# Optimization experiments

Measured on AMD Instinct MI355X. Metric: run time of the kernel, lower is better.

The kernel has to match this reference:

```python
import jax, jax.numpy as jnp
import numpy as np
from jax import lax

D_MODEL = 200
N_LAYER = 12
NHEADS = 8
HEADDIM = 50
D_STATE = 64
D_INNER = 2 * D_MODEL            # 400
CONV_DIM = D_INNER + 2 * D_STATE  # 528 (ngroups=1)
D_IN_PROJ = 2 * D_INNER + 2 * D_STATE + NHEADS  # 936
D_CONV = 4
EPS = 1e-5


def rmsnorm(x, w):
    v = jnp.mean(jnp.square(x), axis=-1, keepdims=True)
    return x * lax.rsqrt(v + EPS) * w


def groupnorm(x, groups, g, b):
    B, C, H, W = x.shape
    xg = x.reshape(B, groups, C // groups, H, W)
    mu = jnp.mean(xg, axis=(2, 3, 4), keepdims=True)
    var = jnp.mean(jnp.square(xg - mu), axis=(2, 3, 4), keepdims=True)
    xn = ((xg - mu) * lax.rsqrt(var + EPS)).reshape(B, C, H, W)
    return xn * g[:, None, None] + b[:, None, None]


def patch_embed(x, pe_conv_w, proj_in_w, gn_g, gn_b, spec_w):
    b, c, l, d = x.shape
    # time path: 'b c l d' -> (b, 1, c*l, d), conv -> (b, 25, c*l, 8)
    time_x = x.reshape(b, 1, c * l, d)
    t = lax.conv_general_dilated(time_x, proj_in_w, (1, 25), ((0, 0), (24, 24)),
                                 dimension_numbers=('NCHW', 'OIHW', 'NCHW'))
    t = jax.nn.gelu(groupnorm(t, 5, gn_g, gn_b), approximate=False)
    time_emb = t.transpose(0, 2, 1, 3).reshape(b, c, l, D_MODEL)
    # freq path: rfft over patch dim, norm='forward'
    spec = jnp.abs(jnp.fft.rfft(x, axis=-1, norm='forward'))  # (b,c,l,101)
    spec_emb = jnp.einsum('bclf,df->bcld', spec, spec_w)
    patch = time_emb + spec_emb
    # depthwise 7x7 positional conv over (d, c, l)
    pos = lax.conv_general_dilated(patch.transpose(0, 3, 1, 2), pe_conv_w, (1, 1),
                                   ((3, 3), (3, 3)),
                                   dimension_numbers=('NCHW', 'OIHW', 'NCHW'),
                                   feature_group_count=D_MODEL)
    return patch + pos.transpose(0, 2, 3, 1)


def ssd_scan(xh, dt, B, C, A, D):
    # xh: (b,l,h,p)  dt: (b,l,h)  B,C: (b,l,n)  A,D: (h,)
    b, l, h, p = xh.shape

    def step(state, inp):
        x_t, dt_t, B_t, C_t = inp
        dA = jnp.exp(dt_t * A)  # (b,h)
        state = state * dA[:, :, None, None] + \
            (dt_t[:, :, None, None] * x_t[:, :, :, None]) * B_t[:, None, None, :]
        y = jnp.einsum('bhpn,bn->bhp', state, C_t)
        return state, y

    state0 = jnp.zeros((b, h, p, D_STATE), xh.dtype)
    _, ys = lax.scan(step, state0,
                     (xh.transpose(1, 0, 2, 3), dt.transpose(1, 0, 2),
                      B.transpose(1, 0, 2), C.transpose(1, 0, 2)))
    return ys.transpose(1, 0, 2, 3) + xh * D[None, None, :, None]


def mamba2(u, in_w, conv_w, conv_b, dt_bias, A_log, D, gn_w, out_w):
    b, l, _ = u.shape
    zxbcdt = u @ in_w.T  # (b,l,936)
    z = zxbcdt[..., :D_INNER]
    xBC = zxbcdt[..., D_INNER:D_INNER + CONV_DIM]
    dt = jax.nn.softplus(zxbcdt[..., D_INNER + CONV_DIM:] + dt_bias)  # (b,l,8)
    # causal depthwise conv1d, kernel 4
    xc = lax.conv_general_dilated(xBC.transpose(0, 2, 1), conv_w, (1,), ((D_CONV - 1, 0),),
                                  dimension_numbers=('NCH', 'OIH', 'NCH'),
                                  feature_group_count=CONV_DIM)
    xBC = jax.nn.silu((xc + conv_b[:, None]).transpose(0, 2, 1))
    x = xBC[..., :D_INNER].reshape(b, l, NHEADS, HEADDIM)
    Bm = xBC[..., D_INNER:D_INNER + D_STATE]
    Cm = xBC[..., D_INNER + D_STATE:]
    y = ssd_scan(x, dt, Bm, Cm, -jnp.exp(A_log), D).reshape(b, l, D_INNER)
    y = rmsnorm(y * jax.nn.silu(z), gn_w)  # RMSNormGated, norm_before_gate=False
    return y @ out_w.T


@jax.checkpoint
def layer(hidden, residual, norm_w, in_w, conv_w, conv_b, dt_bias, A_log, D, gn_w, out_w):
    residual = hidden + residual
    hidden = mamba2(rmsnorm(residual, norm_w), in_w, conv_w, conv_b, dt_bias, A_log, D, gn_w, out_w)
    return hidden, residual


def forward(x, pe_conv_w, proj_in_w, gn_g, gn_b, spec_w, norm_w, in_proj_w, conv_w, conv_b,
            dt_bias, A_log, D, gnorm_w, out_proj_w, norm_f_w, head_w, head_b):
    b, c, l, d = x.shape
    hidden = patch_embed(x, pe_conv_w, proj_in_w, gn_g, gn_b, spec_w).reshape(b, c * l, d)
    residual = jnp.zeros_like(hidden)
    for i in range(N_LAYER):
        hidden, residual = layer(hidden, residual, norm_w[i], in_proj_w[i], conv_w[i],
                                 conv_b[i], dt_bias[i], A_log[i], D[i], gnorm_w[i], out_proj_w[i])
    hidden = rmsnorm(hidden + residual, norm_f_w).reshape(b, c, l, d)
    return hidden @ head_w.T + head_b


def setup_inputs():
    key = jax.random.key(0)
    ks = jax.random.split(key, 12)
    B, CH, L, P = 16, 19, 30, 200

    def g(k, shape, scale):
        return jax.random.normal(k, shape, jnp.float32) * scale

    dt = jax.random.uniform(ks[8], (N_LAYER, NHEADS), jnp.float32, 1e-3, 0.1)
    return {
        'x': g(ks[0], (B, CH, L, P), 1.0),
        'pe_conv_w': g(ks[1], (D_MODEL, 1, 7, 7), 0.15),
        'proj_in_w': g(ks[2], (25, 1, 1, 49), 0.14),
        'gn_g': jnp.ones(25, jnp.float32),
        'gn_b': jnp.zeros(25, jnp.float32),
        'spec_w': g(ks[3], (D_MODEL, 101), 0.1),
        'norm_w': jnp.ones((N_LAYER, D_MODEL), jnp.float32),
        'in_proj_w': g(ks[4], (N_LAYER, D_IN_PROJ, D_MODEL), 0.07),
        'conv_w': g(ks[5], (N_LAYER, CONV_DIM, 1, D_CONV), 0.4),
        'conv_b': jnp.zeros((N_LAYER, CONV_DIM), jnp.float32),
        'dt_bias': jnp.log(jnp.expm1(dt)),
        'A_log': jnp.log(jax.random.uniform(ks[9], (N_LAYER, NHEADS), jnp.float32, 1.0, 16.0)),
        'D': jnp.ones((N_LAYER, NHEADS), jnp.float32),
        'gnorm_w': jnp.ones((N_LAYER, D_INNER), jnp.float32),
        'out_proj_w': g(ks[6], (N_LAYER, D_MODEL, D_INNER), 0.05),
        'norm_f_w': jnp.ones(D_MODEL, jnp.float32),
        'head_w': g(ks[7], (D_MODEL, D_MODEL), 0.07),
        'head_b': jnp.zeros(D_MODEL, jnp.float32),
    }


def reference(x, pe_conv_w, proj_in_w, gn_g, gn_b, spec_w, norm_w, in_proj_w, conv_w, conv_b,
              dt_bias, A_log, D, gnorm_w, out_proj_w, norm_f_w, head_w, head_b):
    return forward(x, pe_conv_w, proj_in_w, gn_g, gn_b, spec_w, norm_w, in_proj_w, conv_w,
                   conv_b, dt_bias, A_log, D, gnorm_w, out_proj_w, norm_f_w, head_w, head_b)
```

## Files before the change

### kernel.cpp

```cpp
#include <hip/hip_runtime.h>
#include <hip/hip_bf16.h>
#include <math.h>

#define D_MODEL   200
#define N_LAYER   12
#define NHEADS    8
#define HEADDIM   50
#define D_STATE   64
#define D_INNER   400
#define CONV_DIM  528
#define D_IN_PROJ 936
#define D_CONV    4
#define EPS       1e-5f

#define BATCH 16
#define CH    19
#define LLEN  30
#define SEQ   570
#define NTOK  9120
#define NFREQ 101

typedef __attribute__((ext_vector_type(8))) short s8v;
typedef __attribute__((ext_vector_type(4))) float f32x4;

__device__ __forceinline__ short f2bf(float f) {
    unsigned u = __float_as_uint(f);
    u += 0x7FFFu + ((u >> 16) & 1u);
    return (short)(u >> 16);
}

__global__ __launch_bounds__(256) void gemm_bf16(
    const short* __restrict__ A, const short* __restrict__ W,
    const float* __restrict__ bias, const float* __restrict__ rowscale,
    float* __restrict__ C, int M, int N, int Kp, int accum)
{
    __shared__ __align__(16) short As[128][40];
    __shared__ __align__(16) short Ws[128][40];

    int bm = blockIdx.y * 128;
    int bn = blockIdx.x * 128;
    int tid = threadIdx.x;
    int lane = tid & 63;
    int wv = tid >> 6;
    int wm = wv & 1, wn = wv >> 1;
    int lm = lane & 15, lg = lane >> 4;

    int sr = tid >> 1;
    int sh_ = (tid & 1) * 16;

    f32x4 acc[4][4];
#pragma unroll
    for (int i = 0; i < 4; i++)
#pragma unroll
        for (int j = 0; j < 4; j++) acc[i][j] = (f32x4)0.f;

    for (int k0 = 0; k0 < Kp; k0 += 32) {
        {
            s8v v0 = (s8v)0, v1 = (s8v)0;
            if (bm + sr < M) {
                const short* ga = A + (size_t)(bm + sr) * Kp + k0 + sh_;
                v0 = *(const s8v*)ga;
                v1 = *(const s8v*)(ga + 8);
            }
            *(s8v*)&As[sr][sh_] = v0;
            *(s8v*)&As[sr][sh_ + 8] = v1;
        }
        {
            s8v v0 = (s8v)0, v1 = (s8v)0;
            if (bn + sr < N) {
                const short* gw = W + (size_t)(bn + sr) * Kp + k0 + sh_;
                v0 = *(const s8v*)gw;
                v1 = *(const s8v*)(gw + 8);
            }
            *(s8v*)&Ws[sr][sh_] = v0;
            *(s8v*)&Ws[sr][sh_ + 8] = v1;
        }
        __syncthreads();

        s8v af[4], bf[4];
#pragma unroll
        for (int i = 0; i < 4; i++)
            af[i] = *(const s8v*)&As[wm * 64 + i * 16 + lm][lg * 8];
#pragma unroll
        for (int j = 0; j < 4; j++)
            bf[j] = *(const s8v*)&Ws[wn * 64 + j * 16 + lm][lg * 8];
#pragma unroll
        for (int i = 0; i < 4; i++)
#pragma unroll
            for (int j = 0; j < 4; j++)
                acc[i][j] = __builtin_amdgcn_mfma_f32_16x16x32_bf16(
                    af[i], bf[j], acc[i][j], 0, 0, 0);
        __syncthreads();
    }

#pragma unroll
    for (int j = 0; j < 4; j++) {
        int n = bn + wn * 64 + j * 16 + lm;
        if (n >= N) continue;
        float bv = bias ? bias[n] : 0.f;
#pragma unroll
        for (int i = 0; i < 4; i++) {
            int mbase = bm + wm * 64 + i * 16 + lg * 4;
#pragma unroll
            for (int r = 0; r < 4; r++) {
                int m = mbase + r;
                if (m >= M) continue;
                size_t idx = (size_t)m * N + n;
                float v = acc[i][j][r];
                if (rowscale) v *= rowscale[m];
                v += bv;
                if (accum) v += C[idx];
                C[idx] = v;
            }
        }
    }
}

__global__ __launch_bounds__(256) void gemm_nt(
    const float* __restrict__ A, const float* __restrict__ W,
    const float* __restrict__ bias, float* __restrict__ C,
    int M, int N, int K, int accum)
{
    const int BM = 128, BK = 16;
    __shared__ float As[16][BM + 4];
    __shared__ float Ws[16][BM + 4];

    int bm = blockIdx.y * BM;
    int bn = blockIdx.x * BM;
    int tid = threadIdx.x;
    int lr = tid >> 1;
    int lc = (tid & 1) * 8;
    int tx = tid & 15;
    int ty = tid >> 4;

    float acc[8][8];
#pragma unroll
    for (int i = 0; i < 8; i++)
#pragma unroll
        for (int j = 0; j < 8; j++) acc[i][j] = 0.f;

    for (int k0 = 0; k0 < K; k0 += BK) {
#pragma unroll
        for (int i = 0; i < 8; i++) {
            int gr = bm + lr, gk = k0 + lc + i;
            As[lc + i][lr] = (gr < M && gk < K) ? A[(size_t)gr * K + gk] : 0.f;
        }
#pragma unroll
        for (int i = 0; i < 8; i++) {
            int gr = bn + lr, gk = k0 + lc + i;
            Ws[lc + i][lr] = (gr < N && gk < K) ? W[(size_t)gr * K + gk] : 0.f;
        }
        __syncthreads();
#pragma unroll
        for (int kk = 0; kk < BK; kk++) {
            float a[8], bv[8];
#pragma unroll
            for (int i = 0; i < 8; i++) a[i] = As[kk][ty * 8 + i];
#pragma unroll
            for (int j = 0; j < 8; j++) bv[j] = Ws[kk][tx * 8 + j];
#pragma unroll
            for (int i = 0; i < 8; i++)
#pragma unroll
                for (int j = 0; j < 8; j++)
                    acc[i][j] = fmaf(a[i], bv[j], acc[i][j]);
        }
        __syncthreads();
    }

#pragma unroll
    for (int i = 0; i < 8; i++) {
        int gm = bm + ty * 8 + i;
        if (gm >= M) continue;
#pragma unroll
        for (int j = 0; j < 8; j++) {
            int gn = bn + tx * 8 + j;
            if (gn >= N) continue;
            float v = acc[i][j];
            if (bias) v += bias[gn];
            if (accum) v += C[(size_t)gm * N + gn];
            C[(size_t)gm * N + gn] = v;
        }
    }
}

__global__ __launch_bounds__(256) void cast_pad_kernel(
    const float* __restrict__ src, short* __restrict__ dst,
    int R, int K, int Kp)
{
    int idx = blockIdx.x * 256 + threadIdx.x;
    if (idx >= R * Kp) return;
    int r = idx / Kp, k = idx - r * Kp;
    dst[idx] = (k < K) ? f2bf(src[(size_t)r * K + k]) : (short)0;
}

__global__ __launch_bounds__(256) void time_conv_kernel(
    const float* __restrict__ x, const float* __restrict__ pw,
    float* __restrict__ traw)
{
    int br = blockIdx.x;
    __shared__ float xr[200];
    if (threadIdx.x < 200) xr[threadIdx.x] = x[(size_t)br * 200 + threadIdx.x];
    __syncthreads();
    if (threadIdx.x < 200) {
        int oc = threadIdx.x >> 3, j = threadIdx.x & 7;
        int start = j * 25 - 24;
        float acc = 0.f;
#pragma unroll
        for (int k = 0; k < 49; k++) {
            int d = start + k;
            if (d >= 0 && d < 200) acc = fmaf(xr[d], pw[oc * 49 + k], acc);
        }
        int b = br / SEQ, row = br % SEQ;
        traw[(((size_t)b * 25 + oc) * SEQ + row) * 8 + j] = acc;
    }
}

__global__ __launch_bounds__(256) void gn_stats_kernel(
    const float* __restrict__ traw, float* __restrict__ stats)
{
    int bg = blockIdx.x;
    int b = bg / 5, g = bg % 5;
    const float* base = traw + ((size_t)b * 25 + g * 5) * SEQ * 8;
    float s = 0.f, q = 0.f;
    for (int i = threadIdx.x; i < 5 * SEQ * 8; i += 256) {
        float v = base[i];
        s += v; q = fmaf(v, v, q);
    }
    __shared__ float rs[4], rq[4];
    int lane = threadIdx.x & 63, w = threadIdx.x >> 6;
#pragma unroll
    for (int o = 32; o; o >>= 1) { s += __shfl_xor(s, o, 64); q += __shfl_xor(q, o, 64); }
    if (lane == 0) { rs[w] = s; rq[w] = q; }
    __syncthreads();
    if (threadIdx.x == 0) {
        float S = rs[0] + rs[1] + rs[2] + rs[3];
        float Q = rq[0] + rq[1] + rq[2] + rq[3];
        float inv = 1.f / (5.f * SEQ * 8.f);
        float mean = S * inv;
        float var = Q * inv - mean * mean;
        stats[bg * 2] = mean;
        stats[bg * 2 + 1] = rsqrtf(var + EPS);
    }
}

__global__ __launch_bounds__(256) void gn_gelu_kernel(
    const float* __restrict__ traw, const float* __restrict__ stats,
    const float* __restrict__ gn_g, const float* __restrict__ gn_b,
    float* __restrict__ patch)
{
    int idx = blockIdx.x * 256 + threadIdx.x;
    if (idx >= NTOK * 200) return;
    int d = idx % 200;
    int row = (idx / 200) % SEQ;
    int b = idx / (200 * SEQ);
    int oc = d >> 3, j = d & 7;
    float v = traw[(((size_t)b * 25 + oc) * SEQ + row) * 8 + j];
    int g = oc / 5;
    float mean = stats[(b * 5 + g) * 2];
    float rstd = stats[(b * 5 + g) * 2 + 1];
    v = (v - mean) * rstd * gn_g[oc] + gn_b[oc];
    float ge = 0.5f * v * (1.f + erff(v * 0.70710678118654752f));
    patch[idx] = ge;
}

__global__ __launch_bounds__(256) void dft_init_kernel(float* __restrict__ CS)
{
    int idx = blockIdx.x * 256 + threadIdx.x;
    if (idx >= 202 * 200) return;
    int f = idx / 200, d = idx % 200;
    int fr = (f < NFREQ) ? f : (f - NFREQ);
    int m = (fr * d) % 200;
    float ang = -6.283185307179586f * (float)m * (1.f / 200.f);
    CS[idx] = (f < NFREQ) ? cosf(ang) : sinf(ang);
}

__global__ __launch_bounds__(256) void dft_init_bf_kernel(short* __restrict__ CS)
{
    int idx = blockIdx.x * 256 + threadIdx.x;
    if (idx >= 202 * 224) return;
    int f = idx / 224, d = idx - f * 224;
    short out = 0;
    if (d < 200) {
        int fr = (f < NFREQ) ? f : (f - NFREQ);
        int m = (fr * d) % 200;
        float ang = -6.283185307179586f * (float)m * (1.f / 200.f);
        out = f2bf((f < NFREQ) ? cosf(ang) : sinf(ang));
    }
    CS[idx] = out;
}

__global__ __launch_bounds__(256) void mag_kernel(
    const float* __restrict__ cs_out, float* __restrict__ magv)
{
    int idx = blockIdx.x * 256 + threadIdx.x;
    if (idx >= NTOK * NFREQ) return;
    int m = idx / NFREQ, f = idx % NFREQ;
    float re = cs_out[(size_t)m * 202 + f];
    float im = cs_out[(size_t)m * 202 + NFREQ + f];
    magv[idx] = sqrtf(re * re + im * im) * 0.005f;
}

__global__ __launch_bounds__(256) void mag_bf_kernel(
    const float* __restrict__ cs_out, short* __restrict__ magv)
{
    int idx = blockIdx.x * 256 + threadIdx.x;
    if (idx >= NTOK * 128) return;
    int m = idx >> 7, f = idx & 127;
    short out = 0;
    if (f < NFREQ) {
        float re = cs_out[(size_t)m * 202 + f];
        float im = cs_out[(size_t)m * 202 + NFREQ + f];
        out = f2bf(sqrtf(re * re + im * im) * 0.005f);
    }
    magv[idx] = out;
}

__global__ __launch_bounds__(256) void pe_conv3_kernel(
    const float* __restrict__ patch, const float* __restrict__ pw,
    float* __restrict__ hidden)
{
    int b = blockIdx.x, dc = blockIdx.y, ct = blockIdx.z;
    int d0 = dc * 16, c0 = ct * 4;
    __shared__ float pl[10 * 30 * 16];
    __shared__ float wl[49 * 16];
    int tid = threadIdx.x;
    int dd = tid & 15;
    int d = d0 + dd;

    for (int i = tid; i < 10 * 30 * 16; i += 256) {
        int ddl = i & 15, r = i >> 4;
        int l = r % 30, cr = r / 30;
        int cc = c0 + cr - 3, dl = d0 + ddl;
        pl[i] = (cc >= 0 && cc < CH && dl < 200)
                    ? patch[((size_t)(b * CH + cc) * LLEN + l) * 200 + dl] : 0.f;
    }
    for (int i = tid; i < 49 * 16; i += 256) {
        int k = i >> 4, dl = d0 + (i & 15);
        wl[i] = (dl < 200) ? pw[(size_t)dl * 49 + k] : 0.f;
    }
    __syncthreads();

    float wreg[49];
#pragma unroll
    for (int k = 0; k < 49; k++) wreg[k] = wl[k * 16 + dd];

    for (int o = tid; o < 4 * 30 * 16; o += 256) {
        int r2 = o >> 4;
        int l = r2 % 30, ci = r2 / 30;
        int c = c0 + ci;
        if (c >= CH) continue;
        float acc = pl[((ci + 3) * 30 + l) * 16 + dd];
#pragma unroll
        for (int i = 0; i < 7; i++) {
#pragma unroll
            for (int j = 0; j < 7; j++) {
                int ll = l + j - 3;
                if (ll < 0 || ll >= LLEN) continue;
                acc = fmaf(pl[((ci + i) * 30 + ll) * 16 + dd], wreg[i * 7 + j], acc);
            }
        }
        if (d < 200) hidden[((size_t)(b * CH + c) * LLEN + l) * 200 + d] = acc;
    }
}

__global__ __launch_bounds__(64) void add_rmsnorm_kernel(
    const float* __restrict__ hidden, float* __restrict__ residual,
    const float* __restrict__ wn, float* __restrict__ u,
    short* __restrict__ ubf, int first)
{
    int m = blockIdx.x;
    int lane = threadIdx.x;
    const float* hr = hidden + (size_t)m * 200;
    float* rr = residual + (size_t)m * 200;
    float v[4];
    float ss = 0.f;
#pragma unroll
    for (int i = 0; i < 4; i++) {
        int k = lane + i * 64;
        float xv = 0.f;
        if (k < 200) {
            xv = hr[k] + (first ? 0.f : rr[k]);
            rr[k] = xv;
        }
        v[i] = xv;
        ss = fmaf(xv, xv, ss);
    }
#pragma unroll
    for (int o = 32; o; o >>= 1) ss += __shfl_xor(ss, o, 64);
    float rstd = rsqrtf(ss * (1.f / 200.f) + EPS);
#pragma unroll
    for (int i = 0; i < 4; i++) {
        int k = lane + i * 64;
        float val = v[i] * rstd * ((k < 200) ? wn[k] : 0.f);
        if (k < 200 && u) u[(size_t)m * 200 + k] = val;
        if (ubf) {
            if (k < 200) ubf[(size_t)m * 224 + k] = f2bf(val);
            else if (k < 224) ubf[(size_t)m * 224 + k] = 0;
        }
    }
}

__global__ __launch_bounds__(256) void norm_dt_kernel(
    const float* __restrict__ hidden, float* __restrict__ residual,
    const float* __restrict__ wn, short* __restrict__ ubf,
    const float* __restrict__ Win, const float* __restrict__ dt_bias,
    float* __restrict__ dtb, int layer, int first)
{
    int m = blockIdx.x;
    int tid = threadIdx.x;
    __shared__ float su[200];
    __shared__ float rs[4];
    float xv = 0.f;
    if (tid < 200) {
        xv = hidden[(size_t)m * 200 + tid] + (first ? 0.f : residual[(size_t)m * 200 + tid]);
        residual[(size_t)m * 200 + tid] = xv;
    }
    float ss = xv * xv;
#pragma unroll
    for (int o = 32; o; o >>= 1) ss += __shfl_xor(ss, o, 64);
    int lane = tid & 63, w = tid >> 6;
    if (lane == 0) rs[w] = ss;
    __syncthreads();
    float rstd = rsqrtf((rs[0] + rs[1] + rs[2] + rs[3]) * (1.f / 200.f) + EPS);
    if (tid < 200) {
        float val = xv * rstd * wn[tid];
        su[tid] = val;
        ubf[(size_t)m * 224 + tid] = f2bf(val);
    } else if (tid < 224) {
        ubf[(size_t)m * 224 + tid] = 0;
    }
    __syncthreads();
    int h = tid >> 5, l = tid & 31;
    const float* wr = Win + (size_t)layer * D_IN_PROJ * 200 + (size_t)(928 + h) * 200;
    float s = 0.f;
    for (int k = l; k < 200; k += 32) s = fmaf(su[k], wr[k], s);
    s += __shfl_xor(s, 16, 32);
    s += __shfl_xor(s, 8, 32);
    s += __shfl_xor(s, 4, 32);
    s += __shfl_xor(s, 2, 32);
    s += __shfl_xor(s, 1, 32);
    if (l == 0) {
        float raw = s + dt_bias[layer * NHEADS + h];
        dtb[(size_t)m * NHEADS + h] = (raw > 20.f) ? raw : log1pf(expf(raw));
    }
}

__global__ __launch_bounds__(256) void dt_gemv_kernel(
    const float* __restrict__ u, const float* __restrict__ Win,
    const float* __restrict__ dt_bias, float* __restrict__ dtb, int layer)
{
    int tid = threadIdx.x;
    int tok = blockIdx.x * 4 + (tid >> 6);
    int head = (tid >> 3) & 7;
    int l8 = tid & 7;
    const float* ur = u + (size_t)tok * 200;
    const float* wr = Win + (size_t)layer * D_IN_PROJ * 200 + (size_t)(928 + head) * 200;
    float s = 0.f;
    for (int k = l8; k < 200; k += 8) s = fmaf(ur[k], wr[k], s);
    s += __shfl_xor(s, 1, 64);
    s += __shfl_xor(s, 2, 64);
    s += __shfl_xor(s, 4, 64);
    if (l8 == 0) {
        float raw = s + dt_bias[layer * NHEADS + head];
        dtb[(size_t)tok * NHEADS + head] = (raw > 20.f) ? raw : log1pf(expf(raw));
    }
}

__global__ __launch_bounds__(256) void dtconv2_kernel(
    const float* __restrict__ zxbcdt, const float* __restrict__ cw,
    const float* __restrict__ cb, float* __restrict__ xBC, int layer)
{
    int b = blockIdx.x, tt = blockIdx.y;
    int t0 = tt * 8;
    __shared__ float zs[11][528];
    const float* cwl = cw + (size_t)layer * CONV_DIM * 4;
    const float* cbl = cb + (size_t)layer * CONV_DIM;
    for (int i = threadIdx.x; i < 11 * 528; i += 256) {
        int r = i / 528, ch = i - r * 528;
        int t = t0 - 3 + r;
        zs[r][ch] = (t >= 0 && t < SEQ)
                        ? zxbcdt[(size_t)(b * SEQ + t) * D_IN_PROJ + D_INNER + ch] : 0.f;
    }
    __syncthreads();
    for (int o = threadIdx.x; o < 8 * 528; o += 256) {
        int tr = o / 528, ch = o - tr * 528;
        int t = t0 + tr;
        if (t >= SEQ) continue;
        float acc = cbl[ch];
#pragma unroll
        for (int k = 0; k < 4; k++)
            acc = fmaf(zs[tr + k][ch], cwl[ch * 4 + k], acc);
        xBC[(size_t)(b * SEQ + t) * CONV_DIM + ch] = acc / (1.f + __expf(-acc));
    }
}

__global__ __launch_bounds__(256) void ssd_state12_kernel(
    const float* __restrict__ xBC, const float* __restrict__ dtb,
    const float* __restrict__ A_log, float* __restrict__ Sbuf,
    float* __restrict__ Pd, int layer, int lchunk, int nchunk)
{
    int b = blockIdx.x, c = blockIdx.y, bz = blockIdx.z;
    int tid = threadIdx.x;
    int w = tid >> 6, lane = tid & 63;
    int h = bz * 4 + w;
    int t0 = c * lchunk;
    float A = -expf(A_log[layer * NHEADS + h]);

    __shared__ __align__(16) short Bt[64 * 64];
    __shared__ __align__(16) short Xw[4][64 * 64];

    for (int i = tid; i < 512; i += 256) ((s8v*)Bt)[i] = (s8v)0;
#pragma unroll
    for (int ww = 0; ww < 4; ww++)
        for (int i = tid; i < 512; i += 256) ((s8v*)Xw[ww])[i] = (s8v)0;
    __syncthreads();

    float dtv = 0.f;
    if (lane < lchunk) dtv = dtb[(size_t)(b * SEQ + t0 + lane) * NHEADS + h];
    float lc = dtv * A;
#pragma unroll
    for (int o = 1; o < 64; o <<= 1) {
        float v = __shfl_up(lc, o, 64);
        if (lane >= o) lc += v;
    }
    float lcTot = __shfl(lc, lchunk - 1, 64);
    float wdec = __expf(lcTot - lc) * dtv;

    for (int idx = tid; idx < lchunk * 64; idx += 256) {
        int s = idx >> 6, n = idx & 63;
        float v = xBC[(size_t)(b * SEQ + t0 + s) * CONV_DIM + D_INNER + n];
        Bt[n * 64 + s] = f2bf(v);
    }
    for (int idx = lane; idx < lchunk * HEADDIM; idx += 64) {
        int s = idx / HEADDIM, p = idx - s * HEADDIM;
        float ws = __shfl(wdec, s, 64);
        float v = xBC[(size_t)(b * SEQ + t0 + s) * CONV_DIM + h * HEADDIM + p] * ws;
        Xw[w][p * 64 + s] = f2bf(v);
    }
    __syncthreads();

    int lm = lane & 15, lg = lane >> 4;
    f32x4 acc[4][4];
#pragma unroll
    for (int i = 0; i < 4; i++)
#pragma unroll
        for (int j = 0; j < 4; j++) acc[i][j] = (f32x4)0.f;

#pragma unroll
    for (int k0 = 0; k0 < 64; k0 += 32) {
        s8v af[4], bf[4];
#pragma unroll
        for (int i = 0; i < 4; i++)
            af[i] = *(const s8v*)&Xw[w][(i * 16 + lm) * 64 + k0 + lg * 8];
#pragma unroll
        for (int j = 0; j < 4; j++)
            bf[j] = *(const s8v*)&Bt[(j * 16 + lm) * 64 + k0 + lg * 8];
#pragma unroll
        for (int i = 0; i < 4; i++)
#pragma unroll
            for (int j = 0; j < 4; j++)
                acc[i][j] = __builtin_amdgcn_mfma_f32_16x16x32_bf16(
                    af[i], bf[j], acc[i][j], 0, 0, 0);
    }

    float* Sb = Sbuf + ((size_t)((b * NHEADS + h) * nchunk + c)) * (HEADDIM * 64);
#pragma unroll
    for (int i = 0; i < 4; i++) {
        int pbase = i * 16 + lg * 4;
#pragma unroll
        for (int r = 0; r < 4; r++) {
            int p = pbase + r;
            if (p >= HEADDIM) continue;
#pragma unroll
            for (int j = 0; j < 4; j++) {
                int n = j * 16 + lm;
                Sb[(size_t)p * 64 + n] = acc[i][j][r];
            }
        }
    }
    if (lane == 0) Pd[(b * NHEADS + h) * nchunk + c] = __expf(lcTot);
}

__global__ __launch_bounds__(512) void ssd_state_kernel(
    const float* __restrict__ xBC, const float* __restrict__ dtb,
    const float* __restrict__ A_log, float* __restrict__ Sbuf,
    float* __restrict__ Pd, int layer, int lchunk, int nchunk)
{
    int b = blockIdx.x, c = blockIdx.y;
    int tid = threadIdx.x;
    int h = tid >> 6, p = tid & 63;
    float A = -expf(A_log[layer * NHEADS + h]);

    __shared__ float sh[2][544];
    int t0 = c * lchunk, tend = t0 + lchunk;

    {
        const float* base = xBC + (size_t)(b * SEQ + t0) * CONV_DIM;
        sh[0][tid] = base[tid];
        if (tid < 24) {
            int e2 = 512 + tid;
            sh[0][e2] = (e2 < 528) ? base[e2]
                                   : dtb[(size_t)(b * SEQ + t0) * NHEADS + (e2 - 528)];
        }
    }
    __syncthreads();

    float s[64];
#pragma unroll
    for (int n = 0; n < 64; n++) s[n] = 0.f;
    float pacc = 1.f;

    for (int t = t0; t < tend; t++) {
        int cur = (t - t0) & 1, nxt = cur ^ 1;
        float pf0 = 0.f, pf1 = 0.f;
        if (t + 1 < tend) {
            const float* base = xBC + (size_t)(b * SEQ + t + 1) * CONV_DIM;
            pf0 = base[tid];
            if (tid < 24) {
                int e2 = 512 + tid;
                pf1 = (e2 < 528) ? base[e2]
                                 : dtb[(size_t)(b * SEQ + t + 1) * NHEADS + (e2 - 528)];
            }
        }
        float dtv = sh[cur][528 + h];
        float xp  = (p < HEADDIM) ? sh[cur][h * HEADDIM + p] : 0.f;
        float dA = __expf(dtv * A);
        float u  = dtv * xp;
        pacc *= dA;
        const float4* B4 = (const float4*)&sh[cur][D_INNER];
#pragma unroll
        for (int n4 = 0; n4 < 16; n4++) {
            float4 bq = B4[n4];
            s[4 * n4 + 0] = fmaf(s[4 * n4 + 0], dA, u * bq.x);
            s[4 * n4 + 1] = fmaf(s[4 * n4 + 1], dA, u * bq.y);
            s[4 * n4 + 2] = fmaf(s[4 * n4 + 2], dA, u * bq.z);
            s[4 * n4 + 3] = fmaf(s[4 * n4 + 3], dA, u * bq.w);
        }
        if (t + 1 < tend) {
            sh[nxt][tid] = pf0;
            if (tid < 24) sh[nxt][512 + tid] = pf1;
        }
        __syncthreads();
    }

    if (p < HEADDIM) {
        float* Sb = Sbuf + ((size_t)((b * NHEADS + h) * nchunk + c)) * (HEADDIM * 64)
                    + p * 64;
#pragma unroll
        for (int n4 = 0; n4 < 16; n4++)
            ((float4*)Sb)[n4] = make_float4(s[4 * n4], s[4 * n4 + 1],
                                            s[4 * n4 + 2], s[4 * n4 + 3]);
    }
    if (p == 0) Pd[(b * NHEADS + h) * nchunk + c] = pacc;
}

__global__ __launch_bounds__(256) void ssd_scan2b_kernel(
    float* __restrict__ Sbuf, const float* __restrict__ Pd, int nchunk)
{
    int bh = blockIdx.x;
    int e = blockIdx.y * 256 + threadIdx.x;
    if (e >= HEADDIM * 64) return;
    float* base = Sbuf + (size_t)bh * nchunk * (HEADDIM * 64) + e;
    const float* pd = Pd + bh * nchunk;
    float cur = 0.f;
    for (int c = 0; c < nchunk; c++) {
        float l = base[(size_t)c * (HEADDIM * 64)];
        base[(size_t)c * (HEADDIM * 64)] = cur;
        cur = fmaf(pd[c], cur, l);
    }
}

__global__ __launch_bounds__(256) void ssd_out7_kernel(
    const float* __restrict__ xBC, const float* __restrict__ dtb,
    const float* __restrict__ zxbcdt, const float* __restrict__ A_log,
    const float* __restrict__ Dv, const float* __restrict__ Sbuf,
    const float* __restrict__ gw, short* __restrict__ ybf,
    float* __restrict__ ssq, int layer, int lchunk, int nchunk)
{
    int b = blockIdx.x, c = blockIdx.y, bz = blockIdx.z;
    int tid = threadIdx.x;
    int hl = tid >> 6, p = tid & 63;
    int h = bz * 4 + hl;
    float A = -expf(A_log[layer * NHEADS + h]);
    float Dh = Dv[layer * NHEADS + h];
    float gval = (p < HEADDIM) ? gw[(size_t)layer * D_INNER + h * HEADDIM + p] : 0.f;

    __shared__ __align__(16) float sBC[4][2][256];
    int t0 = c * lchunk;
    int npairs = lchunk >> 1;

    const float* xb  = xBC + (size_t)(b * SEQ + t0) * CONV_DIM;
    const float* zb  = zxbcdt + (size_t)(b * SEQ + t0) * D_IN_PROJ;
    const float* dtp = dtb + (size_t)(b * SEQ + t0) * NHEADS + h;

    int ldtok = p >> 5;
    int ldf4  = 100 + (p & 31);
    int ldoff = ldtok * 128 + ((p & 31) << 2);

    float4 gv;
    gv = ((const float4*)(xb + (size_t)ldtok * CONV_DIM))[ldf4];
    *(float4*)&sBC[hl][0][ldoff] = gv;
    float nx0 = (p < HEADDIM) ? xb[h * HEADDIM + p] : 0.f;
    float nx1 = (p < HEADDIM) ? xb[CONV_DIM + h * HEADDIM + p] : 0.f;
    float nz0 = (p < HEADDIM) ? zb[h * HEADDIM + p] : 0.f;
    float nz1 = (p < HEADDIM) ? zb[D_IN_PROJ + h * HEADDIM + p] : 0.f;
    float ndt0 = dtp[0];
    float ndt1 = dtp[NHEADS];
    if (npairs > 1)
        gv = ((const float4*)(xb + (size_t)(2 + ldtok) * CONV_DIM))[ldf4];

    float s[64];
    if (p < HEADDIM) {
        const float* Sb = Sbuf + ((size_t)((b * NHEADS + h) * nchunk + c)) * (HEADDIM * 64)
                          + p * 64;
#pragma unroll
        for (int n4 = 0; n4 < 16; n4++) {
            float4 v = ((const float4*)Sb)[n4];
            s[4 * n4] = v.x; s[4 * n4 + 1] = v.y; s[4 * n4 + 2] = v.z; s[4 * n4 + 3] = v.w;
        }
    } else {
#pragma unroll
        for (int n = 0; n < 64; n++) s[n] = 0.f;
    }

    for (int i = 0; i < npairs; i++) {
        int buf = i & 1;
        int t = t0 + 2 * i;
        float x0 = nx0, x1 = nx1, z0 = nz0, z1 = nz1, dt0 = ndt0, dt1 = ndt1;
        if (i + 1 < npairs) {
            *(float4*)&sBC[hl][buf ^ 1][ldoff] = gv;
            const float* xn = xb + (size_t)(2 * (i + 1)) * CONV_DIM;
            const float* zn = zb + (size_t)(2 * (i + 1)) * D_IN_PROJ;
            nx0 = (p < HEADDIM) ? xn[h * HEADDIM + p] : 0.f;
            nx1 = (p < HEADDIM) ? xn[CONV_DIM + h * HEADDIM + p] : 0.f;
            nz0 = (p < HEADDIM) ? zn[h * HEADDIM + p] : 0.f;
            nz1 = (p < HEADDIM) ? zn[D_IN_PROJ + h * HEADDIM + p] : 0.f;
            ndt0 = dtp[(size_t)(2 * (i + 1)) * NHEADS];
            ndt1 = dtp[(size_t)(2 * (i + 1) + 1) * NHEADS];
            if (i + 2 < npairs)
                gv = ((const float4*)(xb + (size_t)(2 * (i + 2) + ldtok) * CONV_DIM))[ldf4];
        }
#pragma unroll
        for (int k = 0; k < 2; k++) {
            float dtv = k ? dt1 : dt0;
            float xp  = k ? x1 : x0;
            float zv  = k ? z1 : z0;
            float dA = __expf(dtv * A);
            float u  = dtv * xp;
            const float4* B4 = (const float4*)&sBC[hl][buf][k * 128];
            const float4* C4 = (const float4*)&sBC[hl][buf][k * 128 + 64];
            float y0 = 0.f, y1 = 0.f, y2 = 0.f, y3 = 0.f;
#pragma unroll
            for (int n4 = 0; n4 < 16; n4++) {
                float4 bq = B4[n4];
                float4 cq = C4[n4];
                float t0v = fmaf(s[4 * n4 + 0], dA, u * bq.x);
                float t1v = fmaf(s[4 * n4 + 1], dA, u * bq.y);
                float t2v = fmaf(s[4 * n4 + 2], dA, u * bq.z);
                float t3v = fmaf(s[4 * n4 + 3], dA, u * bq.w);
                s[4 * n4 + 0] = t0v; s[4 * n4 + 1] = t1v;
                s[4 * n4 + 2] = t2v; s[4 * n4 + 3] = t3v;
                y0 = fmaf(t0v, cq.x, y0);
                y1 = fmaf(t1v, cq.y, y1);
                y2 = fmaf(t2v, cq.z, y2);
                y3 = fmaf(t3v, cq.w, y3);
            }
            float g0 = 0.f;
            if (p < HEADDIM) {
                float yv = fmaf(xp, Dh, (y0 + y1) + (y2 + y3));
                g0 = yv * (zv / (1.f + __expf(-zv)));
            }
            size_t row0 = (size_t)(b * SEQ + t + k) * 416;
            if (p < HEADDIM) {
                ybf[row0 + h * HEADDIM + p] = f2bf(g0 * gval);
            } else {
                int widx = h * 14 + (p - HEADDIM);
                if (widx < 16) ybf[row0 + 400 + widx] = 0;
            }
            float gs0 = g0 * g0;
#pragma unroll
            for (int o = 32; o; o >>= 1) gs0 += __shfl_xor(gs0, o, 64);
            if (p == 0) ssq[(size_t)(b * SEQ + t + k) * NHEADS + h] = gs0;
        }
    }
}

__global__ __launch_bounds__(256) void rstd_kernel(
    const float* __restrict__ ssq, float* __restrict__ rstdb)
{
    int m = blockIdx.x * 256 + threadIdx.x;
    if (m >= NTOK) return;
    const float4* q = (const float4*)(ssq + (size_t)m * NHEADS);
    float4 a = q[0], bq = q[1];
    float tot = ((a.x + a.y) + (a.z + a.w)) + ((bq.x + bq.y) + (bq.z + bq.w));
    rstdb[m] = rsqrtf(tot * (1.f / D_INNER) + EPS);
}

__global__ __launch_bounds__(512) void ssd_out_kernel(
    const float* __restrict__ xBC, const float* __restrict__ dtb,
    const float* __restrict__ A_log, const float* __restrict__ Dv,
    const float* __restrict__ Sbuf, float* __restrict__ y,
    int layer, int lchunk, int nchunk)
{
    int b = blockIdx.x, c = blockIdx.y;
    int tid = threadIdx.x;
    int h = tid >> 6, p = tid & 63;
    float A = -expf(A_log[layer * NHEADS + h]);
    float Dh = Dv[layer * NHEADS + h];

    __shared__ float sh[2][544];
    int t0 = c * lchunk, tend = t0 + lchunk;

    {
        const float* base = xBC + (size_t)(b * SEQ + t0) * CONV_DIM;
        sh[0][tid] = base[tid];
        if (tid < 24) {
            int e2 = 512 + tid;
            sh[0][e2] = (e2 < 528) ? base[e2]
                                   : dtb[(size_t)(b * SEQ + t0) * NHEADS + (e2 - 528)];
        }
    }

    float s[64];
    if (p < HEADDIM) {
        const float* Sb = Sbuf + ((size_t)((b * NHEADS + h) * nchunk + c)) * (HEADDIM * 64)
                          + p * 64;
#pragma unroll
        for (int n4 = 0; n4 < 16; n4++) {
            float4 v = ((const float4*)Sb)[n4];
            s[4 * n4] = v.x; s[4 * n4 + 1] = v.y; s[4 * n4 + 2] = v.z; s[4 * n4 + 3] = v.w;
        }
    } else {
#pragma unroll
        for (int n = 0; n < 64; n++) s[n] = 0.f;
    }
    __syncthreads();

    for (int t = t0; t < tend; t++) {
        int cur = (t - t0) & 1, nxt = cur ^ 1;
        float pf0 = 0.f, pf1 = 0.f;
        if (t + 1 < tend) {
            const float* base = xBC + (size_t)(b * SEQ + t + 1) * CONV_DIM;
            pf0 = base[tid];
            if (tid < 24) {
                int e2 = 512 + tid;
                pf1 = (e2 < 528) ? base[e2]
                                 : dtb[(size_t)(b * SEQ + t + 1) * NHEADS + (e2 - 528)];
            }
        }
        float dtv = sh[cur][528 + h];
        float xp  = (p < HEADDIM) ? sh[cur][h * HEADDIM + p] : 0.f;
        float dA = __expf(dtv * A);
        float u  = dtv * xp;
        const float4* B4 = (const float4*)&sh[cur][D_INNER];
        const float4* C4 = (const float4*)&sh[cur][D_INNER + D_STATE];
        float y0 = 0.f, y1 = 0.f, y2 = 0.f, y3 = 0.f;
#pragma unroll
        for (int n4 = 0; n4 < 16; n4++) {
            float4 bq = B4[n4];
            float4 cq = C4[n4];
            float t0v = fmaf(s[4 * n4 + 0], dA, u * bq.x);
            float t1v = fmaf(s[4 * n4 + 1], dA, u * bq.y);
            float t2v = fmaf(s[4 * n4 + 2], dA, u * bq.z);
            float t3v = fmaf(s[4 * n4 + 3], dA, u * bq.w);
            s[4 * n4 + 0] = t0v; s[4 * n4 + 1] = t1v;
            s[4 * n4 + 2] = t2v; s[4 * n4 + 3] = t3v;
            y0 = fmaf(t0v, cq.x, y0);
            y1 = fmaf(t1v, cq.y, y1);
            y2 = fmaf(t2v, cq.z, y2);
            y3 = fmaf(t3v, cq.w, y3);
        }
        if (p < HEADDIM) {
            float yv = (y0 + y1) + (y2 + y3);
            y[(size_t)(b * SEQ + t) * D_INNER + h * HEADDIM + p] = fmaf(xp, Dh, yv);
        }
        if (t + 1 < tend) {
            sh[nxt][tid] = pf0;
            if (tid < 24) sh[nxt][512 + tid] = pf1;
        }
        __syncthreads();
    }
}

__global__ __launch_bounds__(256) void gate_norm_kernel(
    float* __restrict__ y, const float* __restrict__ zxbcdt,
    const float* __restrict__ gw, short* __restrict__ ybf, int layer)
{
    int m = blockIdx.x;
    __shared__ float buf[D_INNER];
    __shared__ float red[4];
    const float* z = zxbcdt + (size_t)m * D_IN_PROJ;
    float* yr = y + (size_t)m * D_INNER;
    const float* gwl = gw + (size_t)layer * D_INNER;
    float ss = 0.f;
    for (int k = threadIdx.x; k < D_INNER; k += 256) {
        float zv = z[k];
        float sz = zv / (1.f + expf(-zv));
        float g = yr[k] * sz;
        buf[k] = g;
        ss = fmaf(g, g, ss);
    }
    int lane = threadIdx.x & 63, w = threadIdx.x >> 6;
#pragma unroll
    for (int o = 32; o; o >>= 1) ss += __shfl_xor(ss, o, 64);
    if (lane == 0) red[w] = ss;
    __syncthreads();
    float tot = red[0] + red[1] + red[2] + red[3];
    float rstd = rsqrtf(tot * (1.f / D_INNER) + EPS);
    for (int k = threadIdx.x; k < 416; k += 256) {
        if (k < D_INNER) {
            float v = buf[k] * rstd * gwl[k];
            yr[k] = v;
            if (ybf) ybf[(size_t)m * 416 + k] = f2bf(v);
        } else if (ybf) {
            ybf[(size_t)m * 416 + k] = 0;
        }
    }
}

extern "C" void kernel_launch(void* const* d_in, const int* in_sizes, int n_in,
                              void* d_out, int out_size, void* d_ws, size_t ws_size,
                              hipStream_t stream)
{
    const float* x         = (const float*)d_in[0];
    const float* pe_conv_w = (const float*)d_in[1];
    const float* proj_in_w = (const float*)d_in[2];
    const float* gn_g      = (const float*)d_in[3];
    const float* gn_b      = (const float*)d_in[4];
    const float* spec_w    = (const float*)d_in[5];
    const float* norm_w    = (const float*)d_in[6];
    const float* in_proj_w = (const float*)d_in[7];
    const float* conv_w    = (const float*)d_in[8];
    const float* conv_b    = (const float*)d_in[9];
    const float* dt_bias   = (const float*)d_in[10];
    const float* A_log     = (const float*)d_in[11];
    const float* Dv        = (const float*)d_in[12];
    const float* gnorm_w   = (const float*)d_in[13];
    const float* out_proj_w= (const float*)d_in[14];
    const float* norm_f_w  = (const float*)d_in[15];
    const float* head_w    = (const float*)d_in[16];
    const float* head_b    = (const float*)d_in[17];
    float* out = (float*)d_out;
    float* ws  = (float*)d_ws;

    const size_t needA = 28011424ull * sizeof(float);
    int fast = (ws_size >= needA) ? 1 : 0;

    int nchunk, lchunk;
    float *residual = ws, *hidden = ws + 1824000;
    float *zxbcdt, *xBC, *dtb, *Sbuf, *Pd;
    float *ubuf = nullptr, *ybuf = nullptr, *ssq = nullptr, *rstdb = nullptr;
    short *w_in_bf = nullptr, *w_out_bf = nullptr, *w_head_bf = nullptr,
          *w_spec_bf = nullptr, *csmat_bf = nullptr, *x_bf = nullptr,
          *ubuf_bf = nullptr, *ybuf_bf = nullptr, *magb_bf = nullptr;

    if (fast) {
        nchunk = 15; lchunk = 38;
        zxbcdt = ws + 3648000;
        xBC    = ws + 12184320;
        dtb    = ws + 16999680;
        Sbuf   = ws + 17072640;
        Pd     = ws + 23216640;
        short* pool = (short*)(ws + 23218560);
        w_in_bf   = pool;
        w_out_bf  = pool + 2515968;
        w_head_bf = pool + 3514368;
        w_spec_bf = pool + 3559168;
        ubuf_bf   = pool + 3584768;
        ybuf_bf   = pool + 5627648;
        ssq       = ws + 27929344;
        rstdb     = ws + 28002304;
        csmat_bf  = (short*)(Sbuf + 4000000);
        x_bf      = (short*)(Sbuf + 4100000);
        magb_bf   = (short*)(Sbuf + 5200000);
    } else {
        nchunk = 6; lchunk = 95;
        ubuf   = ws + 3648000;
        zxbcdt = ws + 5472000;
        xBC    = ws + 14008320;
        dtb    = ws + 18823680;
        ybuf   = ws + 18896640;
        Sbuf   = ws + 1824000;
        Pd     = ws + 5470000;
    }

    float* traw  = fast ? Sbuf : ybuf;
    float* patch = zxbcdt;
    float* csout = fast ? (Sbuf + 2000000) : (xBC + 50000);
    float* csmat = xBC;
    float* magb  = fast ? nullptr : (xBC + 2000000);
    float* stats = dtb;

    if (fast) {
        cast_pad_kernel<<<(12 * 936 * 224 + 255) / 256, 256, 0, stream>>>(
            in_proj_w, w_in_bf, 12 * 936, 200, 224);
        cast_pad_kernel<<<(12 * 200 * 416 + 255) / 256, 256, 0, stream>>>(
            out_proj_w, w_out_bf, 12 * 200, 400, 416);
        cast_pad_kernel<<<(200 * 224 + 255) / 256, 256, 0, stream>>>(
            head_w, w_head_bf, 200, 200, 224);
        cast_pad_kernel<<<(200 * 128 + 255) / 256, 256, 0, stream>>>(
            spec_w, w_spec_bf, 200, 101, 128);
        cast_pad_kernel<<<(9120 * 224 + 255) / 256, 256, 0, stream>>>(
            x, x_bf, 9120, 200, 224);
        dft_init_bf_kernel<<<(202 * 224 + 255) / 256, 256, 0, stream>>>(csmat_bf);
    } else {
        dft_init_kernel<<<(202 * 200 + 255) / 256, 256, 0, stream>>>(csmat);
    }

    time_conv_kernel<<<NTOK, 256, 0, stream>>>(x, proj_in_w, traw);
    gn_stats_kernel<<<80, 256, 0, stream>>>(traw, stats);
    gn_gelu_kernel<<<(NTOK * 200 + 255) / 256, 256, 0, stream>>>(traw, stats, gn_g, gn_b, patch);
    if (fast) {
        gemm_bf16<<<dim3(2, 72), 256, 0, stream>>>(x_bf, csmat_bf, nullptr, nullptr, csout,
                                                   NTOK, 202, 224, 0);
        mag_bf_kernel<<<(NTOK * 128 + 255) / 256, 256, 0, stream>>>(csout, magb_bf);
        gemm_bf16<<<dim3(2, 72), 256, 0, stream>>>(magb_bf, w_spec_bf, nullptr, nullptr, patch,
                                                   NTOK, 200, 128, 1);
    } else {
        gemm_nt<<<dim3(2, 72), 256, 0, stream>>>(x, csmat, nullptr, csout, NTOK, 202, 200, 0);
        mag_kernel<<<(NTOK * NFREQ + 255) / 256, 256, 0, stream>>>(csout, magb);
        gemm_nt<<<dim3(2, 72), 256, 0, stream>>>(magb, spec_w, nullptr, patch,
                                                 NTOK, 200, NFREQ, 1);
    }
    pe_conv3_kernel<<<dim3(16, 13, 5), 256, 0, stream>>>(patch, pe_conv_w, hidden);

    for (int i = 0; i < N_LAYER; i++) {
        if (fast) {
            norm_dt_kernel<<<NTOK, 256, 0, stream>>>(hidden, residual, norm_w + i * 200,
                                                     ubuf_bf, in_proj_w, dt_bias, dtb,
                                                     i, (i == 0) ? 1 : 0);
            gemm_bf16<<<dim3(8, 72), 256, 0, stream>>>(
                ubuf_bf, w_in_bf + (size_t)i * 936 * 224, nullptr, nullptr, zxbcdt,
                NTOK, D_IN_PROJ, 224, 0);
        } else {
            add_rmsnorm_kernel<<<NTOK, 64, 0, stream>>>(hidden, residual, norm_w + i * 200,
                                                        ubuf, nullptr, (i == 0) ? 1 : 0);
            dt_gemv_kernel<<<NTOK / 4, 256, 0, stream>>>(ubuf, in_proj_w, dt_bias, dtb, i);
            gemm_nt<<<dim3(8, 72), 256, 0, stream>>>(
                ubuf, in_proj_w + (size_t)i * D_IN_PROJ * 200, nullptr, zxbcdt,
                NTOK, D_IN_PROJ, 200, 0);
        }
        dtconv2_kernel<<<dim3(16, 72), 256, 0, stream>>>(zxbcdt, conv_w, conv_b, xBC, i);
        {
            dim3 g(BATCH, nchunk);
            if (fast) {
                ssd_state12_kernel<<<dim3(BATCH, nchunk, 2), 256, 0, stream>>>(
                    xBC, dtb, A_log, Sbuf, Pd, i, lchunk, nchunk);
                ssd_scan2b_kernel<<<dim3(BATCH * NHEADS, 13), 256, 0, stream>>>(Sbuf, Pd, nchunk);
                ssd_out7_kernel<<<dim3(BATCH, nchunk, 2), 256, 0, stream>>>(
                    xBC, dtb, zxbcdt, A_log, Dv, Sbuf, gnorm_w, ybuf_bf, ssq,
                    i, lchunk, nchunk);
                rstd_kernel<<<(NTOK + 255) / 256, 256, 0, stream>>>(ssq, rstdb);
                gemm_bf16<<<dim3(2, 72), 256, 0, stream>>>(
                    ybuf_bf, w_out_bf + (size_t)i * 200 * 416, nullptr, rstdb, hidden,
                    NTOK, 200, 416, 0);
            } else {
                ssd_state_kernel<<<g, 512, 0, stream>>>(xBC, dtb, A_log, Sbuf, Pd,
                                                        i, lchunk, nchunk);
                ssd_scan2b_kernel<<<dim3(BATCH * NHEADS, 13), 256, 0, stream>>>(Sbuf, Pd, nchunk);
                ssd_out_kernel<<<g, 512, 0, stream>>>(xBC, dtb, A_log, Dv, Sbuf, ybuf,
                                                      i, lchunk, nchunk);
                gate_norm_kernel<<<NTOK, 256, 0, stream>>>(ybuf, zxbcdt, gnorm_w, nullptr, i);
                gemm_nt<<<dim3(2, 72), 256, 0, stream>>>(
                    ybuf, out_proj_w + (size_t)i * 200 * D_INNER, nullptr, hidden,
                    NTOK, 200, D_INNER, 0);
            }
        }
    }

    add_rmsnorm_kernel<<<NTOK, 64, 0, stream>>>(hidden, residual, norm_f_w,
                                                fast ? nullptr : ubuf,
                                                fast ? ubuf_bf : nullptr, 0);
    if (fast) {
        gemm_bf16<<<dim3(2, 72), 256, 0, stream>>>(ubuf_bf, w_head_bf, head_b, nullptr, out,
                                                   NTOK, 200, 224, 0);
    } else {
        gemm_nt<<<dim3(2, 72), 256, 0, stream>>>(ubuf, head_w, head_b, out,
                                                 NTOK, 200, 200, 0);
    }
}
```

Baseline: 2.301 ms.

## Rewrite SSD chunk output as bf16 MFMA matmuls instead of sequential scan

Replaces the per-token sequential recurrence in the SSD output kernel with the chunked SSD formulation: compute C·Bᵀ with MFMA, apply a causal decay mask from a prefix sum of dt·A, then multiply by X and add the C·state contribution, all in bf16 MFMA. This removes the serial per-step loop over the chunk in favour of dense matrix ops. It loses precision by casting the state, B, C and X to bf16. The fixed 48-row tiles assume lchunk ≤ 48.

```diff
diff --git a/kernel.cpp b/kernel.cpp
--- a/kernel.cpp
+++ b/kernel.cpp
@@ -670,7 +670,7 @@
     }
 }
 
-__global__ __launch_bounds__(256) void ssd_out7_kernel(
+__global__ __launch_bounds__(256) void ssd_out13_kernel(
     const float* __restrict__ xBC, const float* __restrict__ dtb,
     const float* __restrict__ zxbcdt, const float* __restrict__ A_log,
     const float* __restrict__ Dv, const float* __restrict__ Sbuf,
@@ -679,108 +679,166 @@
 {
     int b = blockIdx.x, c = blockIdx.y, bz = blockIdx.z;
     int tid = threadIdx.x;
-    int hl = tid >> 6, p = tid & 63;
-    int h = bz * 4 + hl;
+    int w = tid >> 6, lane = tid & 63;
+    int h = bz * 4 + w;
+    int t0 = c * lchunk;
     float A = -expf(A_log[layer * NHEADS + h]);
     float Dh = Dv[layer * NHEADS + h];
-    float gval = (p < HEADDIM) ? gw[(size_t)layer * D_INNER + h * HEADDIM + p] : 0.f;
-
-    __shared__ __align__(16) float sBC[4][2][256];
-    int t0 = c * lchunk;
-    int npairs = lchunk >> 1;
-
-    const float* xb  = xBC + (size_t)(b * SEQ + t0) * CONV_DIM;
-    const float* zb  = zxbcdt + (size_t)(b * SEQ + t0) * D_IN_PROJ;
-    const float* dtp = dtb + (size_t)(b * SEQ + t0) * NHEADS + h;
-
-    int ldtok = p >> 5;
-    int ldf4  = 100 + (p & 31);
-    int ldoff = ldtok * 128 + ((p & 31) << 2);
-
-    float4 gv;
-    gv = ((const float4*)(xb + (size_t)ldtok * CONV_DIM))[ldf4];
-    *(float4*)&sBC[hl][0][ldoff] = gv;
-    float nx0 = (p < HEADDIM) ? xb[h * HEADDIM + p] : 0.f;
-    float nx1 = (p < HEADDIM) ? xb[CONV_DIM + h * HEADDIM + p] : 0.f;
-    float nz0 = (p < HEADDIM) ? zb[h * HEADDIM + p] : 0.f;
-    float nz1 = (p < HEADDIM) ? zb[D_IN_PROJ + h * HEADDIM + p] : 0.f;
-    float ndt0 = dtp[0];
-    float ndt1 = dtp[NHEADS];
-    if (npairs > 1)
-        gv = ((const float4*)(xb + (size_t)(2 + ldtok) * CONV_DIM))[ldf4];
-
-    float s[64];
-    if (p < HEADDIM) {
-        const float* Sb = Sbuf + ((size_t)((b * NHEADS + h) * nchunk + c)) * (HEADDIM * 64)
-                          + p * 64;
-#pragma unroll
-        for (int n4 = 0; n4 < 16; n4++) {
-            float4 v = ((const float4*)Sb)[n4];
-            s[4 * n4] = v.x; s[4 * n4 + 1] = v.y; s[4 * n4 + 2] = v.z; s[4 * n4 + 3] = v.w;
-        }
-    } else {
-#pragma unroll
-        for (int n = 0; n < 64; n++) s[n] = 0.f;
-    }
-
-    for (int i = 0; i < npairs; i++) {
-        int buf = i & 1;
-        int t = t0 + 2 * i;
-        float x0 = nx0, x1 = nx1, z0 = nz0, z1 = nz1, dt0 = ndt0, dt1 = ndt1;
-        if (i + 1 < npairs) {
-            *(float4*)&sBC[hl][buf ^ 1][ldoff] = gv;
-            const float* xn = xb + (size_t)(2 * (i + 1)) * CONV_DIM;
-            const float* zn = zb + (size_t)(2 * (i + 1)) * D_IN_PROJ;
-            nx0 = (p < HEADDIM) ? xn[h * HEADDIM + p] : 0.f;
-            nx1 = (p < HEADDIM) ? xn[CONV_DIM + h * HEADDIM + p] : 0.f;
-            nz0 = (p < HEADDIM) ? zn[h * HEADDIM + p] : 0.f;
-            nz1 = (p < HEADDIM) ? zn[D_IN_PROJ + h * HEADDIM + p] : 0.f;
-            ndt0 = dtp[(size_t)(2 * (i + 1)) * NHEADS];
-            ndt1 = dtp[(size_t)(2 * (i + 1) + 1) * NHEADS];
-            if (i + 2 < npairs)
-                gv = ((const float4*)(xb + (size_t)(2 * (i + 2) + ldtok) * CONV_DIM))[ldf4];
-        }
-#pragma unroll
-        for (int k = 0; k < 2; k++) {
-            float dtv = k ? dt1 : dt0;
-            float xp  = k ? x1 : x0;
-            float zv  = k ? z1 : z0;
-            float dA = __expf(dtv * A);
-            float u  = dtv * xp;
-            const float4* B4 = (const float4*)&sBC[hl][buf][k * 128];
-            const float4* C4 = (const float4*)&sBC[hl][buf][k * 128 + 64];
-            float y0 = 0.f, y1 = 0.f, y2 = 0.f, y3 = 0.f;
-#pragma unroll
-            for (int n4 = 0; n4 < 16; n4++) {
-                float4 bq = B4[n4];
-                float4 cq = C4[n4];
-                float t0v = fmaf(s[4 * n4 + 0], dA, u * bq.x);
-                float t1v = fmaf(s[4 * n4 + 1], dA, u * bq.y);
-                float t2v = fmaf(s[4 * n4 + 2], dA, u * bq.z);
-                float t3v = fmaf(s[4 * n4 + 3], dA, u * bq.w);
-                s[4 * n4 + 0] = t0v; s[4 * n4 + 1] = t1v;
-                s[4 * n4 + 2] = t2v; s[4 * n4 + 3] = t3v;
-                y0 = fmaf(t0v, cq.x, y0);
-                y1 = fmaf(t1v, cq.y, y1);
-                y2 = fmaf(t2v, cq.z, y2);
-                y3 = fmaf(t3v, cq.w, y3);
+
+    __shared__ __align__(16) short Ct[64 * 72];
+    __shared__ __align__(16) short Bt[64 * 72];
+    __shared__ __align__(16) short Gm[4][48 * 72];
+    __shared__ __align__(16) short Xt[4][64 * 72];
+    __shared__ __align__(16) short Sn[4][64 * 72];
+
+    for (int i = tid; i < 576; i += 256) { ((s8v*)Ct)[i] = (s8v)0; ((s8v*)Bt)[i] = (s8v)0; }
+#pragma unroll
+    for (int ww = 0; ww < 4; ww++)
+        for (int i = tid; i < 576; i += 256) {
+            ((s8v*)Xt[ww])[i] = (s8v)0; ((s8v*)Sn[ww])[i] = (s8v)0;
+        }
+    __syncthreads();
+
+    float dtv = 0.f;
+    if (lane < lchunk) dtv = dtb[(size_t)(b * SEQ + t0 + lane) * NHEADS + h];
+    float lc = dtv * A;
+#pragma unroll
+    for (int o = 1; o < 64; o <<= 1) {
+        float v = __shfl_up(lc, o, 64);
+        if (lane >= o) lc += v;
+    }
+
+    for (int idx = tid; idx < lchunk * 64; idx += 256) {
+        int s = idx >> 6, n = idx & 63;
+        const float* row = xBC + (size_t)(b * SEQ + t0 + s) * CONV_DIM + D_INNER;
+        Bt[s * 72 + n] = f2bf(row[n]);
+        Ct[s * 72 + n] = f2bf(row[64 + n]);
+    }
+    for (int p = 0; p < HEADDIM; p++) {
+        if (lane < lchunk)
+            Xt[w][p * 72 + lane] =
+                f2bf(xBC[(size_t)(b * SEQ + t0 + lane) * CONV_DIM + h * HEADDIM + p]);
+    }
+    {
+        const float* Sb = Sbuf + ((size_t)((b * NHEADS + h) * nchunk + c)) * (HEADDIM * 64);
+        for (int p = 0; p < HEADDIM; p++)
+            Sn[w][p * 72 + lane] = f2bf(Sb[(size_t)p * 64 + lane]);
+    }
+    __syncthreads();
+
+    int lm = lane & 15, lg = lane >> 4;
+
+    f32x4 acc[3][4];
+#pragma unroll
+    for (int i = 0; i < 3; i++)
+#pragma unroll
+        for (int j = 0; j < 4; j++) acc[i][j] = (f32x4)0.f;
+#pragma unroll
+    for (int k0 = 0; k0 < 64; k0 += 32) {
+        s8v af[3], bfv[4];
+#pragma unroll
+        for (int i = 0; i < 3; i++)
+            af[i] = *(const s8v*)&Ct[(i * 16 + lm) * 72 + k0 + lg * 8];
+#pragma unroll
+        for (int j = 0; j < 4; j++)
+            bfv[j] = *(const s8v*)&Bt[(j * 16 + lm) * 72 + k0 + lg * 8];
+#pragma unroll
+        for (int i = 0; i < 3; i++)
+#pragma unroll
+            for (int j = 0; j < 4; j++)
+                acc[i][j] = __builtin_amdgcn_mfma_f32_16x16x32_bf16(
+                    af[i], bfv[j], acc[i][j], 0, 0, 0);
+    }
+
+    float lcs4[4], dts4[4];
+#pragma unroll
+    for (int j = 0; j < 4; j++) {
+        int s = j * 16 + lm;
+        lcs4[j] = __shfl(lc, s, 64);
+        dts4[j] = __shfl(dtv, s, 64);
+    }
+#pragma unroll
+    for (int i = 0; i < 3; i++) {
+#pragma unroll
+        for (int r = 0; r < 4; r++) {
+            int t = i * 16 + lg * 4 + r;
+            float lct = __shfl(lc, t, 64);
+#pragma unroll
+            for (int j = 0; j < 4; j++) {
+                int s = j * 16 + lm;
+                float gv = (s <= t)
+                    ? acc[i][j][r] * __expf(lct - lcs4[j]) * dts4[j] : 0.f;
+                Gm[w][t * 72 + s] = f2bf(gv);
             }
-            float g0 = 0.f;
-            if (p < HEADDIM) {
-                float yv = fmaf(xp, Dh, (y0 + y1) + (y2 + y3));
-                g0 = yv * (zv / (1.f + __expf(-zv)));
+        }
+    }
+
+    f32x4 acc2[3][4];
+#pragma unroll
+    for (int i = 0; i < 3; i++)
+#pragma unroll
+        for (int j = 0; j < 4; j++) { acc[i][j] = (f32x4)0.f; acc2[i][j] = (f32x4)0.f; }
+#pragma unroll
+    for (int k0 = 0; k0 < 64; k0 += 32) {
+        s8v a1[3], b1[4], a2[3], b2[4];
+#pragma unroll
+        for (int i = 0; i < 3; i++) {
+            a1[i] = *(const s8v*)&Gm[w][(i * 16 + lm) * 72 + k0 + lg * 8];
+            a2[i] = *(const s8v*)&Ct[(i * 16 + lm) * 72 + k0 + lg * 8];
+        }
+#pragma unroll
+        for (int j = 0; j < 4; j++) {
+            b1[j] = *(const s8v*)&Xt[w][(j * 16 + lm) * 72 + k0 + lg * 8];
+            b2[j] = *(const s8v*)&Sn[w][(j * 16 + lm) * 72 + k0 + lg * 8];
+        }
+#pragma unroll
+        for (int i = 0; i < 3; i++)
+#pragma unroll
+            for (int j = 0; j < 4; j++) {
+                acc[i][j]  = __builtin_amdgcn_mfma_f32_16x16x32_bf16(
+                    a1[i], b1[j], acc[i][j], 0, 0, 0);
+                acc2[i][j] = __builtin_amdgcn_mfma_f32_16x16x32_bf16(
+                    a2[i], b2[j], acc2[i][j], 0, 0, 0);
             }
-            size_t row0 = (size_t)(b * SEQ + t + k) * 416;
-            if (p < HEADDIM) {
-                ybf[row0 + h * HEADDIM + p] = f2bf(g0 * gval);
-            } else {
-                int widx = h * 14 + (p - HEADDIM);
-                if (widx < 16) ybf[row0 + 400 + widx] = 0;
+    }
+
+    float gwv[4];
+#pragma unroll
+    for (int j = 0; j < 4; j++) {
+        int p = j * 16 + lm;
+        gwv[j] = (p < HEADDIM) ? gw[(size_t)layer * D_INNER + h * HEADDIM + p] : 0.f;
+    }
+#pragma unroll
+    for (int i = 0; i < 3; i++) {
+#pragma unroll
+        for (int r = 0; r < 4; r++) {
+            int t = i * 16 + lg * 4 + r;
+            float lct = __shfl(lc, t, 64);
+            float elc = __expf(lct);
+            int ok = (t < lchunk);
+            size_t grow = (size_t)(b * SEQ + t0 + t);
+            size_t row0 = grow * 416;
+            float gsum = 0.f;
+#pragma unroll
+            for (int j = 0; j < 4; j++) {
+                int p = j * 16 + lm;
+                float yv = acc[i][j][r] + elc * acc2[i][j][r];
+                float g = 0.f;
+                if (p < HEADDIM && ok) {
+                    float xv = xBC[grow * CONV_DIM + h * HEADDIM + p];
+                    float zv = zxbcdt[grow * D_IN_PROJ + h * HEADDIM + p];
+                    yv += Dh * xv;
+                    g = yv * (zv / (1.f + __expf(-zv)));
+                    ybf[row0 + h * HEADDIM + p] = f2bf(g * gwv[j]);
+                }
+                gsum += g * g;
             }
-            float gs0 = g0 * g0;
-#pragma unroll
-            for (int o = 32; o; o >>= 1) gs0 += __shfl_xor(gs0, o, 64);
-            if (p == 0) ssq[(size_t)(b * SEQ + t + k) * NHEADS + h] = gs0;
+            gsum += __shfl_xor(gsum, 1, 64);
+            gsum += __shfl_xor(gsum, 2, 64);
+            gsum += __shfl_xor(gsum, 4, 64);
+            gsum += __shfl_xor(gsum, 8, 64);
+            if (lm == 0 && ok) ssq[grow * NHEADS + h] = gsum;
+            if (bz == 0 && w == 0 && ok) ybf[row0 + 400 + lm] = 0;
         }
     }
 }
@@ -1047,7 +1105,7 @@
                 ssd_state12_kernel<<<dim3(BATCH, nchunk, 2), 256, 0, stream>>>(
                     xBC, dtb, A_log, Sbuf, Pd, i, lchunk, nchunk);
                 ssd_scan2b_kernel<<<dim3(BATCH * NHEADS, 13), 256, 0, stream>>>(Sbuf, Pd, nchunk);
-                ssd_out7_kernel<<<dim3(BATCH, nchunk, 2), 256, 0, stream>>>(
+                ssd_out13_kernel<<<dim3(BATCH, nchunk, 2), 256, 0, stream>>>(
                     xBC, dtb, zxbcdt, A_log, Dv, Sbuf, gnorm_w, ybuf_bf, ssq,
                     i, lchunk, nchunk);
                 rstd_kernel<<<(NTOK + 255) / 256, 256, 0, stream>>>(ssq, rstdb);
```

Result: no change. 2.290 ms (-0.5%).
